# Optimization experiments

Hardware: AMD Instinct MI355X
Metric: run time of the kernel (lower is better)

The kernel has to match this reference:

```python
import jax, jax.numpy as jnp
import numpy as np
from jax.scipy.special import logsumexp

B, N = 256, 65536
NEG_INF = jnp.float32(-1e30)  # acts as -inf for logsumexp, keeps grads finite


def setup_inputs() -> dict:
    key = jax.random.key(0)
    k1, k2 = jax.random.split(key)
    sim = jax.random.uniform(k1, (B, N), dtype=jnp.float32)
    label = jax.random.uniform(k2, (B, N), dtype=jnp.float32)
    return {"sim": sim, "label": label}


def _ranking_loss(sim, label):
    m = 0.2
    gamma = 64.0
    delta_p = 1.0 - m  # 0.8
    delta_n = m        # 0.2

    pos_mask = label > 0.5
    neg_mask = label < 0.25

    # ---- positives: logit_p = -relu(0.8 - sim).detach() * (sim - 0.8) * gamma ----
    alpha_p = jax.lax.stop_gradient(jnp.maximum(0.8 - sim, 0.0))
    logit_p = -alpha_p * (sim - delta_p) * gamma
    lse_p = logsumexp(jnp.where(pos_mask, logit_p, NEG_INF), axis=1)
    # torch fallback: no positives -> logit_p = [0.0], logsumexp == 0
    lse_p = jnp.where(pos_mask.any(axis=1), lse_p, 0.0)

    # ---- negatives: if >20 negatives, keep only top-10 largest sims ----
    alpha_n_all = jax.lax.stop_gradient(jnp.maximum(sim - 0.2, 0.0))
    logit_n_all = alpha_n_all * (sim - delta_n) * gamma
    lse_n_all = logsumexp(jnp.where(neg_mask, logit_n_all, NEG_INF), axis=1)

    neg_sim_masked = jnp.where(neg_mask, sim, NEG_INF)
    top_v, _ = jax.lax.top_k(neg_sim_masked, 10)  # [B, 10]
    alpha_n_top = jax.lax.stop_gradient(jnp.maximum(top_v - 0.2, 0.0))
    logit_n_top = alpha_n_top * (top_v - delta_n) * gamma
    lse_n_top = logsumexp(logit_n_top, axis=1)

    n_neg = neg_mask.sum(axis=1)
    lse_n = jnp.where(n_neg > 20, lse_n_top, lse_n_all)

    loss_loc = jax.nn.softplus(lse_n + lse_p).sum()
    return loss_loc / sim.shape[0]  # reduction='mean'


def reference(sim, label):
    return _ranking_loss(sim, label)
```

## Files before the change

kernel.cpp:

```cpp
#include <hip/hip_runtime.h>
#include <cmath>

#define NEG_INF (-1.0e30f)

static constexpr int B = 256;
static constexpr int N = 65536;
static constexpr int THREADS = 1024;
static constexpr float C_OFF = 40.96f;

__device__ __forceinline__ float wave_sum_f(float v) {
#pragma unroll
  for (int off = 32; off >= 1; off >>= 1) v += __shfl_xor(v, off, 64);
  return v;
}
__device__ __forceinline__ int wave_sum_i(int v) {
#pragma unroll
  for (int off = 32; off >= 1; off >>= 1) v += __shfl_xor(v, off, 64);
  return v;
}

__device__ __forceinline__ void merge_lists_shfl(float t[16], int off) {
  float b[16];
#pragma unroll
  for (int i = 0; i < 16; ++i) b[i] = __shfl_xor(t[i], off, 64);
  float c[16];
#pragma unroll
  for (int i = 0; i < 16; ++i) c[i] = fmaxf(t[i], b[15 - i]);
#pragma unroll
  for (int s = 8; s >= 1; s >>= 1) {
#pragma unroll
    for (int i = 0; i < 16; ++i) {
      if ((i & s) == 0) {
        float lo = c[i], hi = c[i + s];
        c[i] = fmaxf(lo, hi);
        c[i + s] = fminf(lo, hi);
      }
    }
  }
#pragma unroll
  for (int i = 0; i < 16; ++i) t[i] = c[i];
}

__device__ __forceinline__ void process_elem(float s, float l, float& s_p,
                                             float& s_n, int& nn, float t[16]) {
  const bool pos = l > 0.5f;
  const bool neg = l < 0.25f;
  float dp = 0.8f - s;
  float lp = (dp > 0.f) ? 64.f * dp * dp : 0.f;
  float dn = s - 0.2f;
  float ln_ = (dn > 0.f) ? 64.f * dn * dn : 0.f;
  float arg = pos ? (lp - C_OFF) : (neg ? (ln_ - C_OFF) : -1.0e30f);
  float e = __expf(arg);
  if (pos) s_p += e;
  if (neg) {
    s_n += e;
    ++nn;
    if (s > t[9]) {
      t[9] = s;
#pragma unroll
      for (int i = 9; i > 0; --i) {
        float a = t[i - 1], bb = t[i];
        t[i - 1] = fmaxf(a, bb);
        t[i] = fminf(a, bb);
      }
    }
  }
}

__global__ void __launch_bounds__(THREADS) ranking_row_kernel(
    const float* __restrict__ sim, const float* __restrict__ label,
    float* __restrict__ row_loss) {
  const int row = blockIdx.x;
  const int tid = threadIdx.x;
  const float4* sim4 = reinterpret_cast<const float4*>(sim) + (size_t)row * (N / 4);
  const float4* lab4 = reinterpret_cast<const float4*>(label) + (size_t)row * (N / 4);

  float s_p = 0.f, s_n = 0.f;
  int nn = 0;
  float t[16];
#pragma unroll
  for (int i = 0; i < 16; ++i) t[i] = NEG_INF;

  constexpr int ITER = N / 4 / THREADS;
#pragma unroll 4
  for (int it = 0; it < ITER; ++it) {
    float4 sv = sim4[it * THREADS + tid];
    float4 lv = lab4[it * THREADS + tid];
    process_elem(sv.x, lv.x, s_p, s_n, nn, t);
    process_elem(sv.y, lv.y, s_p, s_n, nn, t);
    process_elem(sv.z, lv.z, s_p, s_n, nn, t);
    process_elem(sv.w, lv.w, s_p, s_n, nn, t);
  }

  s_p = wave_sum_f(s_p);
  s_n = wave_sum_f(s_n);
  nn = wave_sum_i(nn);
#pragma unroll
  for (int off = 1; off < 64; off <<= 1) merge_lists_shfl(t, off);

  __shared__ float ls_p[16], ls_n[16];
  __shared__ int ls_c[16];
  __shared__ float ltop[16][16];
  const int wave = tid >> 6, lane = tid & 63;
  if (lane == 0) {
    ls_p[wave] = s_p;
    ls_n[wave] = s_n;
    ls_c[wave] = nn;
#pragma unroll
    for (int i = 0; i < 16; ++i) ltop[wave][i] = t[i];
  }
  __syncthreads();

  if (wave == 0) {
    float m[16];
    if (lane < 16) {
#pragma unroll
      for (int i = 0; i < 16; ++i) m[i] = ltop[lane][i];
    } else {
#pragma unroll
      for (int i = 0; i < 16; ++i) m[i] = NEG_INF;
    }
    merge_lists_shfl(m, 1);
    merge_lists_shfl(m, 2);
    merge_lists_shfl(m, 4);
    merge_lists_shfl(m, 8);

    float sp = (lane < 16) ? ls_p[lane] : 0.f;
    float sn = (lane < 16) ? ls_n[lane] : 0.f;
    int cn = (lane < 16) ? ls_c[lane] : 0;
    sp = wave_sum_f(sp);
    sn = wave_sum_f(sn);
    cn = wave_sum_i(cn);

    if (lane == 0) {
      float lse_p = (sp > 0.f) ? (C_OFF + __logf(sp)) : 0.f;
      float lse_n_all = (sn > 0.f) ? (C_OFF + __logf(sn)) : NEG_INF;

      float mx = NEG_INF;
      float lg[10];
#pragma unroll
      for (int i = 0; i < 10; ++i) {
        float v = m[i];
        float a = fmaxf(v - 0.2f, 0.f);
        float lo = a * (v - 0.2f) * 64.f;
        lg[i] = lo;
        mx = fmaxf(mx, lo);
      }
      float ss = 0.f;
#pragma unroll
      for (int i = 0; i < 10; ++i) ss += __expf(lg[i] - mx);
      float lse_n_top = mx + __logf(ss);

      float lse_n = (cn > 20) ? lse_n_top : lse_n_all;
      float x = lse_n + lse_p;
      float loss = fmaxf(x, 0.f) + log1pf(__expf(-fabsf(x)));
      row_loss[row] = loss;
    }
  }
}

__global__ void __launch_bounds__(256) final_reduce_kernel(
    const float* __restrict__ row_loss, float* __restrict__ out) {
  const int tid = threadIdx.x;
  float v = row_loss[tid];
  v = wave_sum_f(v);
  __shared__ float ws[4];
  if ((tid & 63) == 0) ws[tid >> 6] = v;
  __syncthreads();
  if (tid == 0) out[0] = (ws[0] + ws[1] + ws[2] + ws[3]) * (1.0f / 256.0f);
}

extern "C" void kernel_launch(void* const* d_in, const int* in_sizes, int n_in,
                              void* d_out, int out_size, void* d_ws, size_t ws_size,
                              hipStream_t stream) {
  const float* sim = (const float*)d_in[0];
  const float* label = (const float*)d_in[1];
  float* out = (float*)d_out;
  float* rows = (float*)d_ws;
  ranking_row_kernel<<<dim3(B), dim3(THREADS), 0, stream>>>(sim, label, rows);
  final_reduce_kernel<<<dim3(1), dim3(256), 0, stream>>>(rows, out);
}
```

Baseline: 150.8 us.

## Split each row across two blocks and combine partials in final kernel

Each row is now processed by two 1024-thread blocks instead of one, giving 512 blocks on the GPU. Each block writes partial sums, a negative count and a top-16 list to workspace, and the final kernel merges the two halves per row before computing the loss. The per-element math is also simplified to a single select, fmax and fma, and the loop is fully unrolled with an occupancy hint in the launch bounds. The intent is better CU occupancy and load balance on a 256-CU part, at the cost of extra workspace traffic and a heavier combine step.

```diff
diff --git a/kernel.cpp b/kernel.cpp
--- a/kernel.cpp
+++ b/kernel.cpp
@@ -6,6 +6,7 @@
 static constexpr int B = 256;
 static constexpr int N = 65536;
 static constexpr int THREADS = 1024;
+static constexpr int SPLIT = 2;
 static constexpr float C_OFF = 40.96f;
 
 __device__ __forceinline__ float wave_sum_f(float v) {
@@ -41,15 +42,32 @@
   for (int i = 0; i < 16; ++i) t[i] = c[i];
 }
 
+__device__ __forceinline__ void merge_lists_local(float a[16], const float b[16]) {
+  float c[16];
+#pragma unroll
+  for (int i = 0; i < 16; ++i) c[i] = fmaxf(a[i], b[15 - i]);
+#pragma unroll
+  for (int s = 8; s >= 1; s >>= 1) {
+#pragma unroll
+    for (int i = 0; i < 16; ++i) {
+      if ((i & s) == 0) {
+        float lo = c[i], hi = c[i + s];
+        c[i] = fmaxf(lo, hi);
+        c[i + s] = fminf(lo, hi);
+      }
+    }
+  }
+#pragma unroll
+  for (int i = 0; i < 16; ++i) a[i] = c[i];
+}
+
 __device__ __forceinline__ void process_elem(float s, float l, float& s_p,
                                              float& s_n, int& nn, float t[16]) {
   const bool pos = l > 0.5f;
   const bool neg = l < 0.25f;
-  float dp = 0.8f - s;
-  float lp = (dp > 0.f) ? 64.f * dp * dp : 0.f;
-  float dn = s - 0.2f;
-  float ln_ = (dn > 0.f) ? 64.f * dn * dn : 0.f;
-  float arg = pos ? (lp - C_OFF) : (neg ? (ln_ - C_OFF) : -1.0e30f);
+  float d = pos ? (0.8f - s) : (s - 0.2f);
+  float r = fmaxf(d, 0.f);
+  float arg = __builtin_fmaf(64.f * r, r, -C_OFF);
   float e = __expf(arg);
   if (pos) s_p += e;
   if (neg) {
@@ -67,13 +85,17 @@
   }
 }
 
-__global__ void __launch_bounds__(THREADS) ranking_row_kernel(
+__global__ void __launch_bounds__(THREADS, 8) ranking_partial_kernel(
     const float* __restrict__ sim, const float* __restrict__ label,
-    float* __restrict__ row_loss) {
-  const int row = blockIdx.x;
+    float* __restrict__ ws_sp, float* __restrict__ ws_sn,
+    int* __restrict__ ws_cnt, float* __restrict__ ws_top) {
+  const int blk = blockIdx.x;
+  const int row = blk >> 1;
+  const int half = blk & 1;
   const int tid = threadIdx.x;
-  const float4* sim4 = reinterpret_cast<const float4*>(sim) + (size_t)row * (N / 4);
-  const float4* lab4 = reinterpret_cast<const float4*>(label) + (size_t)row * (N / 4);
+  const size_t base4 = (size_t)row * (N / 4) + (size_t)half * (N / (4 * SPLIT));
+  const float4* sim4 = reinterpret_cast<const float4*>(sim) + base4;
+  const float4* lab4 = reinterpret_cast<const float4*>(label) + base4;
 
   float s_p = 0.f, s_n = 0.f;
   int nn = 0;
@@ -81,8 +103,8 @@
 #pragma unroll
   for (int i = 0; i < 16; ++i) t[i] = NEG_INF;
 
-  constexpr int ITER = N / 4 / THREADS;
-#pragma unroll 4
+  constexpr int ITER = N / 4 / THREADS / SPLIT;
+#pragma unroll
   for (int it = 0; it < ITER; ++it) {
     float4 sv = sim4[it * THREADS + tid];
     float4 lv = lab4[it * THREADS + tid];
@@ -133,41 +155,60 @@
     cn = wave_sum_i(cn);
 
     if (lane == 0) {
-      float lse_p = (sp > 0.f) ? (C_OFF + __logf(sp)) : 0.f;
-      float lse_n_all = (sn > 0.f) ? (C_OFF + __logf(sn)) : NEG_INF;
-
-      float mx = NEG_INF;
-      float lg[10];
-#pragma unroll
-      for (int i = 0; i < 10; ++i) {
-        float v = m[i];
-        float a = fmaxf(v - 0.2f, 0.f);
-        float lo = a * (v - 0.2f) * 64.f;
-        lg[i] = lo;
-        mx = fmaxf(mx, lo);
-      }
-      float ss = 0.f;
-#pragma unroll
-      for (int i = 0; i < 10; ++i) ss += __expf(lg[i] - mx);
-      float lse_n_top = mx + __logf(ss);
-
-      float lse_n = (cn > 20) ? lse_n_top : lse_n_all;
-      float x = lse_n + lse_p;
-      float loss = fmaxf(x, 0.f) + log1pf(__expf(-fabsf(x)));
-      row_loss[row] = loss;
-    }
-  }
-}
-
-__global__ void __launch_bounds__(256) final_reduce_kernel(
-    const float* __restrict__ row_loss, float* __restrict__ out) {
-  const int tid = threadIdx.x;
-  float v = row_loss[tid];
-  v = wave_sum_f(v);
-  __shared__ float ws[4];
-  if ((tid & 63) == 0) ws[tid >> 6] = v;
+      ws_sp[blk] = sp;
+      ws_sn[blk] = sn;
+      ws_cnt[blk] = cn;
+#pragma unroll
+      for (int i = 0; i < 16; ++i) ws_top[blk * 16 + i] = m[i];
+    }
+  }
+}
+
+__global__ void __launch_bounds__(256) combine_kernel(
+    const float* __restrict__ ws_sp, const float* __restrict__ ws_sn,
+    const int* __restrict__ ws_cnt, const float* __restrict__ ws_top,
+    float* __restrict__ out) {
+  const int r = threadIdx.x;
+  const int p0 = r * 2, p1 = r * 2 + 1;
+
+  float a[16], b[16];
+#pragma unroll
+  for (int i = 0; i < 16; ++i) a[i] = ws_top[p0 * 16 + i];
+#pragma unroll
+  for (int i = 0; i < 16; ++i) b[i] = ws_top[p1 * 16 + i];
+  merge_lists_local(a, b);
+
+  float sp = ws_sp[p0] + ws_sp[p1];
+  float sn = ws_sn[p0] + ws_sn[p1];
+  int cn = ws_cnt[p0] + ws_cnt[p1];
+
+  float lse_p = (sp > 0.f) ? (C_OFF + __logf(sp)) : 0.f;
+  float lse_n_all = (sn > 0.f) ? (C_OFF + __logf(sn)) : NEG_INF;
+
+  float mx = NEG_INF;
+  float lg[10];
+#pragma unroll
+  for (int i = 0; i < 10; ++i) {
+    float v = a[i];
+    float al = fmaxf(v - 0.2f, 0.f);
+    float lo = al * (v - 0.2f) * 64.f;
+    lg[i] = lo;
+    mx = fmaxf(mx, lo);
+  }
+  float ss = 0.f;
+#pragma unroll
+  for (int i = 0; i < 10; ++i) ss += __expf(lg[i] - mx);
+  float lse_n_top = mx + __logf(ss);
+
+  float lse_n = (cn > 20) ? lse_n_top : lse_n_all;
+  float x = lse_n + lse_p;
+  float loss = fmaxf(x, 0.f) + log1pf(__expf(-fabsf(x)));
+
+  float v = wave_sum_f(loss);
+  __shared__ float wsh[4];
+  if ((r & 63) == 0) wsh[r >> 6] = v;
   __syncthreads();
-  if (tid == 0) out[0] = (ws[0] + ws[1] + ws[2] + ws[3]) * (1.0f / 256.0f);
+  if (r == 0) out[0] = (wsh[0] + wsh[1] + wsh[2] + wsh[3]) * (1.0f / 256.0f);
 }
 
 extern "C" void kernel_launch(void* const* d_in, const int* in_sizes, int n_in,
@@ -176,7 +217,15 @@
   const float* sim = (const float*)d_in[0];
   const float* label = (const float*)d_in[1];
   float* out = (float*)d_out;
-  float* rows = (float*)d_ws;
-  ranking_row_kernel<<<dim3(B), dim3(THREADS), 0, stream>>>(sim, label, rows);
-  final_reduce_kernel<<<dim3(1), dim3(256), 0, stream>>>(rows, out);
-}
+
+  float* wsf = (float*)d_ws;
+  float* ws_sp = wsf;
+  float* ws_sn = wsf + 512;
+  float* ws_top = wsf + 1024;
+  int* ws_cnt = (int*)(wsf + 1024 + 512 * 16);
+
+  ranking_partial_kernel<<<dim3(B * SPLIT), dim3(THREADS), 0, stream>>>(
+      sim, label, ws_sp, ws_sn, ws_cnt, ws_top);
+  combine_kernel<<<dim3(1), dim3(256), 0, stream>>>(ws_sp, ws_sn, ws_cnt, ws_top,
+                                                    out);
+}
```

Result: slower. 162.7 us (+7.9%).
